# Optimization experiments

Measured on AMD Instinct MI355X. Metric: run time of the kernel, lower is better.

The kernel has to match this reference:

```python
import jax, jax.numpy as jnp
import numpy as np

B, S, D = 4, 2048, 1024

def setup_inputs() -> dict:
    key = jax.random.key(0)
    kv, kk, kq, kw = jax.random.split(key, 4)
    scale = 1.0 / np.sqrt(D)
    v = jax.random.normal(kv, (B, S, D), dtype=jnp.float32)
    k = jax.random.normal(kk, (B, S, D), dtype=jnp.float32)
    q = jax.random.normal(kq, (B, S, D), dtype=jnp.float32)
    wi = jax.random.normal(kw, (D, D), dtype=jnp.float32) * scale
    mask = jnp.tril(jnp.ones((S, S), dtype=bool))[None, :, :]  # causal [1,S,S]
    return {"v": v, "k": k, "q": q, "wi": wi, "mask": mask}

def reference(v, k, q, wi, mask):
    # project q, k, v with the shared weight wi
    q = q @ wi
    k = k @ wi
    v = v @ wi
    # scaled dot-product scores [B,S,S]
    scores = jnp.einsum('bqd,bkd->bqk', q, k) / jnp.sqrt(jnp.asarray(q.shape[-1], q.dtype))
    scores = jnp.where(mask, scores, jnp.asarray(-1e10, scores.dtype))
    attn = jax.nn.softmax(scores, axis=-1)
    # residual: q + attn @ v
    return q + jnp.einsum('bqk,bkd->bqd', attn, v)
```

## Files before the change

kernel.cpp:

```cpp
#include <hip/hip_runtime.h>
#include <hip/hip_bf16.h>

typedef __hip_bfloat16 bf16;
typedef short bf16x8 __attribute__((ext_vector_type(8)));
typedef float f32x4 __attribute__((ext_vector_type(4)));

#define HT 16384

__device__ __forceinline__ void gload16(const void* g, void* l) {
    __builtin_amdgcn_global_load_lds(
        (const __attribute__((address_space(1))) void*)g,
        (__attribute__((address_space(3))) void*)l, 16, 0, 0);
}

__device__ __forceinline__ void stage_half(char* lds, const bf16* src, int ld,
                                           int rowbase, int k0, int slotIdx,
                                           int tid)
{
    char* dst = lds + (size_t)slotIdx * HT + tid * 16;
    const int sub = tid >> 3;
    const int cb  = ((tid & 7) ^ (sub & 7)) << 4;
    #pragma unroll
    for (int p = 0; p < 2; ++p) {
        const int row = p * 64 + sub;
        const char* g = (const char*)(src + (size_t)(rowbase + row) * ld + k0) + cb;
        gload16(g, dst + p * 8192);
    }
}

__device__ __forceinline__ void stage_q(char* lds, const bf16* src, int ld,
                                        int rowbase, int k0, int slotIdx,
                                        int tid)
{
    char* dst = lds + (size_t)slotIdx * HT + tid * 16;
    #pragma unroll
    for (int p = 0; p < 4; ++p) {
        const int s = p * 256 + tid;
        const int row = s >> 3;
        const int cb = ((s & 7) ^ (row & 7)) << 4;
        const char* g = (const char*)(src + (size_t)(rowbase + row) * ld + k0) + cb;
        gload16(g, dst + p * 4096);
    }
}

__device__ __forceinline__ bf16x8 ldsfrag(const char* lds, int slotIdx,
                                          int row, int ks, int cb0)
{
    return *(const bf16x8*)(lds + (size_t)slotIdx * HT
                            + row * 128 + (cb0 ^ (ks << 6)));
}

__device__ __forceinline__ float bf2f(short s) {
    union { float f; unsigned u; } c;
    c.u = ((unsigned)(unsigned short)s) << 16;
    return c.f;
}

__launch_bounds__(512, 2)
__global__ void proj_2ph(const bf16* __restrict__ A, const bf16* __restrict__ B,
                         bf16* __restrict__ C)
{
    extern __shared__ char lds[];
    const int orig = blockIdx.y * 8 + blockIdx.x;
    const int wk2 = (orig & 7) * 96 + (orig >> 3);
    const int bi = wk2 >> 3, bj = wk2 & 7;
    const int brow = bi * 256, bcol = bj * 128;

    const int tid  = threadIdx.x;
    const int lane = tid & 63;
    const int w    = tid >> 6;
    const int wm   = w >> 1, wn = w & 1;
    const int fr   = lane & 15, fq = lane >> 4;
    const int cb0  = ((fr & 7) ^ fq) << 4;
    const int hA   = wm >> 1;
    const int rA   = (wm & 1) * 64;
    const int rB   = wn * 64;
    const int NT   = 16;

    f32x4 acc[4][4] = {};
    bf16x8 af[4][2], bv[4][2];

    stage_half(lds, A, 1024, brow,       0, 0, tid);
    stage_half(lds, A, 1024, brow + 128, 0, 1, tid);
    stage_half(lds, B, 1024, bcol,       0, 6, tid);
    stage_half(lds, A, 1024, brow,      64, 2, tid);
    stage_half(lds, A, 1024, brow + 128,64, 3, tid);
    stage_half(lds, B, 1024, bcol,     64, 7, tid);
    asm volatile("s_waitcnt vmcnt(6)" ::: "memory");
    __builtin_amdgcn_s_barrier();

#define MF8(n0)                                                               \
    _Pragma("unroll") for (int m = 0; m < 4; ++m)                             \
    _Pragma("unroll") for (int dn = 0; dn < 2; ++dn)                          \
    _Pragma("unroll") for (int ks = 0; ks < 2; ++ks)                          \
        acc[m][(n0)+dn] = __builtin_amdgcn_mfma_f32_16x16x32_bf16(            \
            af[m][ks], bv[(n0)+dn][ks], acc[m][(n0)+dn], 0, 0, 0);

    for (int t = 0; t < NT; ++t) {
        const int aslot = (t % 3) * 2 + hA;
        const int bslot = 6 + (t & 1);
        const int a2    = ((t + 2) % 3) * 2;
        const int k2    = min(t + 2, NT - 1) << 6;

        #pragma unroll
        for (int m = 0; m < 4; ++m)
            #pragma unroll
            for (int ks = 0; ks < 2; ++ks)
                af[m][ks] = ldsfrag(lds, aslot, rA + m * 16 + fr, ks, cb0);
        #pragma unroll
        for (int n = 0; n < 4; ++n)
            #pragma unroll
            for (int ks = 0; ks < 2; ++ks)
                bv[n][ks] = ldsfrag(lds, bslot, rB + n * 16 + fr, ks, cb0);
        stage_half(lds, A, 1024, brow,       k2, a2,     tid);
        stage_half(lds, A, 1024, brow + 128, k2, a2 + 1, tid);
        __builtin_amdgcn_s_barrier();
        __builtin_amdgcn_s_setprio(1);
        MF8(0)
        __builtin_amdgcn_s_setprio(0);
        __builtin_amdgcn_s_barrier();

        stage_half(lds, B, 1024, bcol, k2, bslot, tid);
        __builtin_amdgcn_s_barrier();
        __builtin_amdgcn_s_setprio(1);
        MF8(2)
        __builtin_amdgcn_s_setprio(0);
        asm volatile("s_waitcnt vmcnt(6)" ::: "memory");
        __builtin_amdgcn_s_barrier();
    }
#undef MF8

    #pragma unroll
    for (int mf = 0; mf < 4; ++mf) {
        const int r0 = brow + wm * 64 + mf * 16 + fq * 4;
        #pragma unroll
        for (int nf = 0; nf < 4; ++nf) {
            const int c = bcol + wn * 64 + nf * 16 + fr;
            #pragma unroll
            for (int j = 0; j < 4; ++j)
                C[(size_t)(r0 + j) * 1024 + c] = __float2bfloat16(acc[mf][nf][j]);
        }
    }
}

template<int MODE>
__device__ __forceinline__ void tile128v2(char* lds, const bf16* A, const bf16* B,
                                          bf16* Cb, float* Cf, const bf16* Res,
                                          int lda, int ldb, int ldcb,
                                          int brow, int bcol, int NT, float scale,
                                          int tid)
{
    const int lane = tid & 63;
    const int w    = tid >> 6;
    const int wm   = w >> 1, wn = w & 1;
    const int fr   = lane & 15, fq = lane >> 4;
    const int cb0  = ((fr & 7) ^ fq) << 4;

    f32x4 acc[4][4] = {};
    bf16x8 af[4][2], bv[4][2];

    stage_q(lds, A, lda, brow, 0,  0, tid);
    stage_q(lds, B, ldb, bcol, 0,  3, tid);
    stage_q(lds, A, lda, brow, 64, 1, tid);
    stage_q(lds, B, ldb, bcol, 64, 4, tid);
    asm volatile("s_waitcnt vmcnt(8)" ::: "memory");
    __builtin_amdgcn_s_barrier();

    for (int t = 0; t < NT; ++t) {
        const int aslot = t % 3, bslot = 3 + (t & 1);
        const int k2 = min(t + 2, NT - 1) << 6;

        #pragma unroll
        for (int m = 0; m < 4; ++m)
            #pragma unroll
            for (int ks = 0; ks < 2; ++ks)
                af[m][ks] = ldsfrag(lds, aslot, wm * 64 + m * 16 + fr, ks, cb0);
        #pragma unroll
        for (int n = 0; n < 4; ++n)
            #pragma unroll
            for (int ks = 0; ks < 2; ++ks)
                bv[n][ks] = ldsfrag(lds, bslot, wn * 64 + n * 16 + fr, ks, cb0);
        stage_q(lds, A, lda, brow, k2, (t + 2) % 3, tid);
        __builtin_amdgcn_s_barrier();
        __builtin_amdgcn_s_setprio(1);
        #pragma unroll
        for (int m = 0; m < 4; ++m)
            #pragma unroll
            for (int n = 0; n < 2; ++n)
                #pragma unroll
                for (int ks = 0; ks < 2; ++ks)
                    acc[m][n] = __builtin_amdgcn_mfma_f32_16x16x32_bf16(
                        af[m][ks], bv[n][ks], acc[m][n], 0, 0, 0);
        __builtin_amdgcn_s_setprio(0);
        __builtin_amdgcn_s_barrier();

        stage_q(lds, B, ldb, bcol, k2, bslot, tid);
        __builtin_amdgcn_s_barrier();
        __builtin_amdgcn_s_setprio(1);
        #pragma unroll
        for (int m = 0; m < 4; ++m)
            #pragma unroll
            for (int n = 2; n < 4; ++n)
                #pragma unroll
                for (int ks = 0; ks < 2; ++ks)
                    acc[m][n] = __builtin_amdgcn_mfma_f32_16x16x32_bf16(
                        af[m][ks], bv[n][ks], acc[m][n], 0, 0, 0);
        __builtin_amdgcn_s_setprio(0);
        asm volatile("s_waitcnt vmcnt(8)" ::: "memory");
        __builtin_amdgcn_s_barrier();
    }

    #pragma unroll
    for (int mf = 0; mf < 4; ++mf) {
        const int r0 = brow + wm * 64 + mf * 16 + fq * 4;
        #pragma unroll
        for (int nf = 0; nf < 4; ++nf) {
            const int c = bcol + wn * 64 + nf * 16 + fr;
            #pragma unroll
            for (int j = 0; j < 4; ++j) {
                if (MODE == 1)
                    Cb[(size_t)(r0 + j) * ldcb + c] =
                        __float2bfloat16(acc[mf][nf][j] * scale);
                else
                    Cf[(size_t)(r0 + j) * ldcb + c] = acc[mf][nf][j] +
                        __bfloat162float(Res[(size_t)(r0 + j) * ldcb + c]);
            }
        }
    }
}

__launch_bounds__(256, 2)
__global__ void scores128(const bf16* __restrict__ qp, const bf16* __restrict__ kp,
                          bf16* __restrict__ P)
{
    extern __shared__ char lds[];
    const int j = blockIdx.x;
    int bi = (int)((__fsqrt_rn(8.0f * j + 1.0f) - 1.0f) * 0.5f);
    while ((bi + 1) * (bi + 2) / 2 <= j) ++bi;
    while (bi * (bi + 1) / 2 > j) --bi;
    const int bj = j - bi * (bi + 1) / 2;
    const int bz = blockIdx.z;

    tile128v2<1>(lds,
                 qp + (size_t)bz * 2048 * 1024,
                 kp + (size_t)bz * 2048 * 1024,
                 P + (size_t)bz * 2048 * 2048, nullptr, nullptr,
                 1024, 1024, 2048,
                 bi * 128, bj * 128, 16, 0.03125f, threadIdx.x);
}

__launch_bounds__(256, 2)
__global__ void pv128(const bf16* __restrict__ P, const bf16* __restrict__ V,
                      const bf16* __restrict__ R, float* __restrict__ C)
{
    extern __shared__ char lds[];
    const int x  = blockIdx.x;
    const int u  = x & 255;
    const int bs = u & 7;
    const int bj = (u >> 3) & 7;
    const int bz = u >> 6;
    const int bi = (x >> 8) ? (15 - bs) : bs;

    tile128v2<2>(lds,
                 P + (size_t)bz * 2048 * 2048,
                 V + (size_t)bz * 1024 * 2048,
                 nullptr,
                 C + (size_t)bz * 2048 * 1024,
                 R + (size_t)bz * 2048 * 1024,
                 2048, 2048, 1024,
                 bi * 128, bj * 128, 2 * (bi + 1), 1.0f, threadIdx.x);
}

__global__ void convert_and_wi(const float* __restrict__ q,
                               const float* __restrict__ k,
                               const float* __restrict__ v,
                               const float* __restrict__ wi,
                               bf16* __restrict__ Xb, bf16* __restrict__ Wt)
{
    __shared__ float t[32][33];
    if (blockIdx.x < 1024) {
        const int n0 = (blockIdx.x & 31) * 32, k0 = (blockIdx.x >> 5) * 32;
        const int lx = threadIdx.x & 31, ly = threadIdx.x >> 5;
        for (int i = ly; i < 32; i += 8)
            t[i][lx] = wi[(size_t)(k0 + i) * 1024 + n0 + lx];
        __syncthreads();
        for (int i = ly; i < 32; i += 8)
            Wt[(size_t)(n0 + i) * 1024 + k0 + lx] = __float2bfloat16(t[lx][i]);
        return;
    }
    const int N8 = 8192 * 1024 / 8;
    const int total = 3 * N8;
    const int nconv = gridDim.x - 1024;
    for (int i = (blockIdx.x - 1024) * 256 + threadIdx.x; i < total;
         i += nconv * 256) {
        const int ti = i / N8, j = i - ti * N8;
        const float4* s = (ti == 0) ? (const float4*)q
                        : (ti == 1) ? (const float4*)k : (const float4*)v;
        float4 a = s[2 * j], bq = s[2 * j + 1];
        float vals[8] = {a.x, a.y, a.z, a.w, bq.x, bq.y, bq.z, bq.w};
        union { short h[8]; bf16x8 v8; } o;
        #pragma unroll
        for (int e = 0; e < 8; ++e) {
            bf16 hh = __float2bfloat16(vals[e]);
            o.h[e] = *(short*)&hh;
        }
        ((bf16x8*)Xb)[i] = o.v8;
    }
}

__global__ void transpose_vp(const bf16* __restrict__ vp, bf16* __restrict__ vpT)
{
    __shared__ bf16 t[32][33];
    const int b = blockIdx.z;
    const int d0 = blockIdx.x * 32, s0 = blockIdx.y * 32;
    const bf16* src = vp + (size_t)b * 2048 * 1024;
    bf16* dst = vpT + (size_t)b * 1024 * 2048;
    const int lx = threadIdx.x & 31, ly = threadIdx.x >> 5;
    for (int i = ly; i < 32; i += 8)
        t[i][lx] = src[(size_t)(s0 + i) * 1024 + d0 + lx];
    __syncthreads();
    for (int i = ly; i < 32; i += 8)
        dst[(size_t)(d0 + i) * 2048 + s0 + lx] = t[lx][i];
}

__launch_bounds__(256)
__global__ void softmax_rows(bf16* __restrict__ P)
{
    const int wid = threadIdx.x >> 6, lane = threadIdx.x & 63;
    const int r = blockIdx.x * 4 + wid, b = blockIdx.y;
    bf16* row = P + ((size_t)b * 2048 + r) * 2048;
    const int nv  = r + 1;
    const int rup = (r & ~127) + 128;

    float vals[4][8];
    float m = -1e30f;
    #pragma unroll
    for (int c = 0; c < 4; ++c) {
        const int k0 = c * 512 + lane * 8;
        if (k0 < rup) {
            bf16x8 x = *(const bf16x8*)(row + k0);
            #pragma unroll
            for (int j = 0; j < 8; ++j) {
                float f = (k0 + j < nv) ? bf2f(x[j]) : -1e30f;
                vals[c][j] = f;
                m = fmaxf(m, f);
            }
        } else {
            #pragma unroll
            for (int j = 0; j < 8; ++j) vals[c][j] = -1e30f;
        }
    }
    #pragma unroll
    for (int o = 32; o; o >>= 1) m = fmaxf(m, __shfl_xor(m, o));

    float sum = 0.f;
    #pragma unroll
    for (int c = 0; c < 4; ++c)
        #pragma unroll
        for (int j = 0; j < 8; ++j) {
            float e = __expf(vals[c][j] - m);
            vals[c][j] = e;
            sum += e;
        }
    #pragma unroll
    for (int o = 32; o; o >>= 1) sum += __shfl_xor(sum, o);
    const float inv = 1.0f / sum;

    #pragma unroll
    for (int c = 0; c < 4; ++c) {
        const int k0 = c * 512 + lane * 8;
        if (k0 < rup) {
            union { short h[8]; bf16x8 v8; } o;
            #pragma unroll
            for (int j = 0; j < 8; ++j) {
                bf16 hh = __float2bfloat16(vals[c][j] * inv);
                o.h[j] = *(short*)&hh;
            }
            *(bf16x8*)(row + k0) = o.v8;
        }
    }
}

extern "C" void kernel_launch(void* const* d_in, const int* in_sizes, int n_in,
                              void* d_out, int out_size, void* d_ws, size_t ws_size,
                              hipStream_t stream)
{
    const float* v  = (const float*)d_in[0];
    const float* k  = (const float*)d_in[1];
    const float* q  = (const float*)d_in[2];
    const float* wi = (const float*)d_in[3];
    float* out = (float*)d_out;

    char* ws = (char*)d_ws;
    const size_t WT_OFF   = 0;
    const size_t PROJ_OFF = WT_OFF + (2u << 20);
    const size_t VPT_OFF  = PROJ_OFF + (size_t)24576 * 1024 * 2;
    const size_t XB_OFF   = VPT_OFF + (size_t)4 * 1024 * 2048 * 2;

    bf16* Wt   = (bf16*)(ws + WT_OFF);
    bf16* proj = (bf16*)(ws + PROJ_OFF);
    bf16* vpT  = (bf16*)(ws + VPT_OFF);
    bf16* Xb   = (bf16*)(ws + XB_OFF);
    bf16* P    = Xb;

    bf16* qp_b = proj;
    bf16* kp_b = proj + (size_t)8192 * 1024;
    bf16* vp_b = proj + (size_t)16384 * 1024;

    (void)hipFuncSetAttribute((const void*)proj_2ph,
            hipFuncAttributeMaxDynamicSharedMemorySize, 131072);
    (void)hipFuncSetAttribute((const void*)scores128,
            hipFuncAttributeMaxDynamicSharedMemorySize, 81920);
    (void)hipFuncSetAttribute((const void*)pv128,
            hipFuncAttributeMaxDynamicSharedMemorySize, 81920);

    convert_and_wi<<<3072, 256, 0, stream>>>(q, k, v, wi, Xb, Wt);

    proj_2ph<<<dim3(8, 96), 512, 131072, stream>>>(Xb, Wt, proj);

    transpose_vp<<<dim3(32, 64, 4), 256, 0, stream>>>(vp_b, vpT);

    scores128<<<dim3(136, 1, 4), 256, 81920, stream>>>(qp_b, kp_b, P);

    softmax_rows<<<dim3(512, 4), 256, 0, stream>>>(P);

    pv128<<<dim3(512), 256, 81920, stream>>>(P, vpT, qp_b, out);
}
```

Baseline: 179.1 us.

## Reassociate attention with shared weight: precompute Wi·Wiᵀ and apply Wi after PV

Uses the shared projection to rewrite the math. Scores become q·(Wi Wiᵀ)·kᵀ, so only a 1024x1024 Gram product and one q projection are computed instead of projecting q, k and v. The output becomes (q + attn·v)·Wi, so the residual and PV run on raw inputs and a final GEMM applies Wi. This removes one of the three large projection GEMMs and the projected-v transpose, and the new transpose kernel converts v directly from fp32. The cost is an extra small GEMM and an extra intermediate Y rounded to bf16, which changes the rounding behaviour.

```diff
diff --git a/kernel.cpp b/kernel.cpp
--- a/kernel.cpp
+++ b/kernel.cpp
@@ -56,14 +56,18 @@
     return c.f;
 }
 
+template<int MODE>
 __launch_bounds__(512, 2)
-__global__ void proj_2ph(const bf16* __restrict__ A, const bf16* __restrict__ B,
-                         bf16* __restrict__ C)
+__global__ void gemm_a256(const bf16* __restrict__ A, const bf16* __restrict__ B,
+                          bf16* __restrict__ Cb, float* __restrict__ Cf)
 {
     extern __shared__ char lds[];
-    const int orig = blockIdx.y * 8 + blockIdx.x;
-    const int wk2 = (orig & 7) * 96 + (orig >> 3);
-    const int bi = wk2 >> 3, bj = wk2 & 7;
+    const int gx = gridDim.x;
+    const int nwg = gx * gridDim.y;
+    const int chunk = nwg >> 3;
+    const int orig = blockIdx.y * gx + blockIdx.x;
+    const int wk2 = (orig & 7) * chunk + (orig >> 3);
+    const int bi = wk2 / gx, bj = wk2 % gx;
     const int brow = bi * 256, bcol = bj * 128;
 
     const int tid  = threadIdx.x;
@@ -137,15 +141,20 @@
         for (int nf = 0; nf < 4; ++nf) {
             const int c = bcol + wn * 64 + nf * 16 + fr;
             #pragma unroll
-            for (int j = 0; j < 4; ++j)
-                C[(size_t)(r0 + j) * 1024 + c] = __float2bfloat16(acc[mf][nf][j]);
+            for (int j = 0; j < 4; ++j) {
+                if (MODE == 0)
+                    Cb[(size_t)(r0 + j) * 1024 + c] =
+                        __float2bfloat16(acc[mf][nf][j]);
+                else
+                    Cf[(size_t)(r0 + j) * 1024 + c] = acc[mf][nf][j];
+            }
         }
     }
 }
 
 template<int MODE>
 __device__ __forceinline__ void tile128v2(char* lds, const bf16* A, const bf16* B,
-                                          bf16* Cb, float* Cf, const bf16* Res,
+                                          bf16* Cb, const float* Rf,
                                           int lda, int ldb, int ldcb,
                                           int brow, int bcol, int NT, float scale,
                                           int tid)
@@ -222,15 +231,15 @@
                     Cb[(size_t)(r0 + j) * ldcb + c] =
                         __float2bfloat16(acc[mf][nf][j] * scale);
                 else
-                    Cf[(size_t)(r0 + j) * ldcb + c] = acc[mf][nf][j] +
-                        __bfloat162float(Res[(size_t)(r0 + j) * ldcb + c]);
+                    Cb[(size_t)(r0 + j) * ldcb + c] = __float2bfloat16(
+                        acc[mf][nf][j] + Rf[(size_t)(r0 + j) * ldcb + c]);
             }
         }
     }
 }
 
 __launch_bounds__(256, 2)
-__global__ void scores128(const bf16* __restrict__ qp, const bf16* __restrict__ kp,
+__global__ void scores128(const bf16* __restrict__ qG, const bf16* __restrict__ kb,
                           bf16* __restrict__ P)
 {
     extern __shared__ char lds[];
@@ -242,16 +251,16 @@
     const int bz = blockIdx.z;
 
     tile128v2<1>(lds,
-                 qp + (size_t)bz * 2048 * 1024,
-                 kp + (size_t)bz * 2048 * 1024,
-                 P + (size_t)bz * 2048 * 2048, nullptr, nullptr,
+                 qG + (size_t)bz * 2048 * 1024,
+                 kb + (size_t)bz * 2048 * 1024,
+                 P + (size_t)bz * 2048 * 2048, nullptr,
                  1024, 1024, 2048,
                  bi * 128, bj * 128, 16, 0.03125f, threadIdx.x);
 }
 
 __launch_bounds__(256, 2)
-__global__ void pv128(const bf16* __restrict__ P, const bf16* __restrict__ V,
-                      const bf16* __restrict__ R, float* __restrict__ C)
+__global__ void pv128(const bf16* __restrict__ P, const bf16* __restrict__ vT,
+                      const float* __restrict__ q, bf16* __restrict__ Y)
 {
     extern __shared__ char lds[];
     const int x  = blockIdx.x;
@@ -263,64 +272,65 @@
 
     tile128v2<2>(lds,
                  P + (size_t)bz * 2048 * 2048,
-                 V + (size_t)bz * 1024 * 2048,
-                 nullptr,
-                 C + (size_t)bz * 2048 * 1024,
-                 R + (size_t)bz * 2048 * 1024,
+                 vT + (size_t)bz * 1024 * 2048,
+                 Y + (size_t)bz * 2048 * 1024,
+                 q + (size_t)bz * 2048 * 1024,
                  2048, 2048, 1024,
                  bi * 128, bj * 128, 2 * (bi + 1), 1.0f, threadIdx.x);
 }
 
-__global__ void convert_and_wi(const float* __restrict__ q,
-                               const float* __restrict__ k,
-                               const float* __restrict__ v,
-                               const float* __restrict__ wi,
-                               bf16* __restrict__ Xb, bf16* __restrict__ Wt)
+__global__ void convert_qk_w(const float* __restrict__ q, const float* __restrict__ k,
+                             const float* __restrict__ wi,
+                             bf16* __restrict__ qb, bf16* __restrict__ kb,
+                             bf16* __restrict__ Wb)
+{
+    const int N8 = 8192 * 1024 / 8;
+    const int W8 = 1024 * 1024 / 8;
+    const int total = 2 * N8 + W8;
+    for (int i = blockIdx.x * 256 + threadIdx.x; i < total; i += gridDim.x * 256) {
+        const float4* s;
+        bf16* dst;
+        int j;
+        if (i < N8)            { s = (const float4*)q;  dst = qb; j = i; }
+        else if (i < 2 * N8)   { s = (const float4*)k;  dst = kb; j = i - N8; }
+        else                   { s = (const float4*)wi; dst = Wb; j = i - 2 * N8; }
+        float4 a = s[2 * j], b = s[2 * j + 1];
+        float vals[8] = {a.x, a.y, a.z, a.w, b.x, b.y, b.z, b.w};
+        union { short h[8]; bf16x8 v8; } o;
+        #pragma unroll
+        for (int e = 0; e < 8; ++e) {
+            bf16 hh = __float2bfloat16(vals[e]);
+            o.h[e] = *(short*)&hh;
+        }
+        ((bf16x8*)dst)[j] = o.v8;
+    }
+}
+
+__global__ void transpose_vwi(const float* __restrict__ v,
+                              const float* __restrict__ wi,
+                              bf16* __restrict__ vT, bf16* __restrict__ Wt)
 {
     __shared__ float t[32][33];
-    if (blockIdx.x < 1024) {
-        const int n0 = (blockIdx.x & 31) * 32, k0 = (blockIdx.x >> 5) * 32;
-        const int lx = threadIdx.x & 31, ly = threadIdx.x >> 5;
+    const int z = blockIdx.z;
+    const int lx = threadIdx.x & 31, ly = threadIdx.x >> 5;
+    if (z < 4) {
+        const int d0 = blockIdx.x * 32, s0 = blockIdx.y * 32;
+        const float* src = v + (size_t)z * 2048 * 1024;
+        bf16* dst = vT + (size_t)z * 1024 * 2048;
+        for (int i = ly; i < 32; i += 8)
+            t[i][lx] = src[(size_t)(s0 + i) * 1024 + d0 + lx];
+        __syncthreads();
+        for (int i = ly; i < 32; i += 8)
+            dst[(size_t)(d0 + i) * 2048 + s0 + lx] = __float2bfloat16(t[lx][i]);
+    } else {
+        if (blockIdx.y >= 32) return;
+        const int n0 = blockIdx.x * 32, k0 = blockIdx.y * 32;
         for (int i = ly; i < 32; i += 8)
             t[i][lx] = wi[(size_t)(k0 + i) * 1024 + n0 + lx];
         __syncthreads();
         for (int i = ly; i < 32; i += 8)
             Wt[(size_t)(n0 + i) * 1024 + k0 + lx] = __float2bfloat16(t[lx][i]);
-        return;
-    }
-    const int N8 = 8192 * 1024 / 8;
-    const int total = 3 * N8;
-    const int nconv = gridDim.x - 1024;
-    for (int i = (blockIdx.x - 1024) * 256 + threadIdx.x; i < total;
-         i += nconv * 256) {
-        const int ti = i / N8, j = i - ti * N8;
-        const float4* s = (ti == 0) ? (const float4*)q
-                        : (ti == 1) ? (const float4*)k : (const float4*)v;
-        float4 a = s[2 * j], bq = s[2 * j + 1];
-        float vals[8] = {a.x, a.y, a.z, a.w, bq.x, bq.y, bq.z, bq.w};
-        union { short h[8]; bf16x8 v8; } o;
-        #pragma unroll
-        for (int e = 0; e < 8; ++e) {
-            bf16 hh = __float2bfloat16(vals[e]);
-            o.h[e] = *(short*)&hh;
-        }
-        ((bf16x8*)Xb)[i] = o.v8;
-    }
-}
-
-__global__ void transpose_vp(const bf16* __restrict__ vp, bf16* __restrict__ vpT)
-{
-    __shared__ bf16 t[32][33];
-    const int b = blockIdx.z;
-    const int d0 = blockIdx.x * 32, s0 = blockIdx.y * 32;
-    const bf16* src = vp + (size_t)b * 2048 * 1024;
-    bf16* dst = vpT + (size_t)b * 1024 * 2048;
-    const int lx = threadIdx.x & 31, ly = threadIdx.x >> 5;
-    for (int i = ly; i < 32; i += 8)
-        t[i][lx] = src[(size_t)(s0 + i) * 1024 + d0 + lx];
-    __syncthreads();
-    for (int i = ly; i < 32; i += 8)
-        dst[(size_t)(d0 + i) * 2048 + s0 + lx] = t[lx][i];
+    }
 }
 
 __launch_bounds__(256)
@@ -392,37 +402,38 @@
     float* out = (float*)d_out;
 
     char* ws = (char*)d_ws;
-    const size_t WT_OFF   = 0;
-    const size_t PROJ_OFF = WT_OFF + (2u << 20);
-    const size_t VPT_OFF  = PROJ_OFF + (size_t)24576 * 1024 * 2;
-    const size_t XB_OFF   = VPT_OFF + (size_t)4 * 1024 * 2048 * 2;
-
-    bf16* Wt   = (bf16*)(ws + WT_OFF);
-    bf16* proj = (bf16*)(ws + PROJ_OFF);
-    bf16* vpT  = (bf16*)(ws + VPT_OFF);
-    bf16* Xb   = (bf16*)(ws + XB_OFF);
-    bf16* P    = Xb;
-
-    bf16* qp_b = proj;
-    bf16* kp_b = proj + (size_t)8192 * 1024;
-    bf16* vp_b = proj + (size_t)16384 * 1024;
-
-    (void)hipFuncSetAttribute((const void*)proj_2ph,
+    const size_t MB = 1u << 20;
+    bf16* Wb = (bf16*)(ws);
+    bf16* Wt = (bf16*)(ws + 2 * MB);
+    bf16* G  = (bf16*)(ws + 4 * MB);
+    bf16* qb = (bf16*)(ws + 6 * MB);
+    bf16* kb = (bf16*)(ws + 22 * MB);
+    bf16* vT = (bf16*)(ws + 38 * MB);
+    bf16* qG = (bf16*)(ws + 54 * MB);
+    bf16* Y  = (bf16*)(ws + 70 * MB);
+    bf16* P  = (bf16*)(ws + 86 * MB);
+
+    (void)hipFuncSetAttribute((const void*)gemm_a256<0>,
+            hipFuncAttributeMaxDynamicSharedMemorySize, 131072);
+    (void)hipFuncSetAttribute((const void*)gemm_a256<2>,
             hipFuncAttributeMaxDynamicSharedMemorySize, 131072);
     (void)hipFuncSetAttribute((const void*)scores128,
             hipFuncAttributeMaxDynamicSharedMemorySize, 81920);
     (void)hipFuncSetAttribute((const void*)pv128,
             hipFuncAttributeMaxDynamicSharedMemorySize, 81920);
 
-    convert_and_wi<<<3072, 256, 0, stream>>>(q, k, v, wi, Xb, Wt);
-
-    proj_2ph<<<dim3(8, 96), 512, 131072, stream>>>(Xb, Wt, proj);
-
-    transpose_vp<<<dim3(32, 64, 4), 256, 0, stream>>>(vp_b, vpT);
-
-    scores128<<<dim3(136, 1, 4), 256, 81920, stream>>>(qp_b, kp_b, P);
+    convert_qk_w<<<2048, 256, 0, stream>>>(q, k, wi, qb, kb, Wb);
+    transpose_vwi<<<dim3(32, 64, 5), 256, 0, stream>>>(v, wi, vT, Wt);
+
+    gemm_a256<0><<<dim3(8, 4), 512, 131072, stream>>>(Wb, Wb, G, nullptr);
+
+    gemm_a256<0><<<dim3(8, 32), 512, 131072, stream>>>(qb, G, qG, nullptr);
+
+    scores128<<<dim3(136, 1, 4), 256, 81920, stream>>>(qG, kb, P);
 
     softmax_rows<<<dim3(512, 4), 256, 0, stream>>>(P);
 
-    pv128<<<dim3(512), 256, 81920, stream>>>(P, vpT, qp_b, out);
-}
+    pv128<<<dim3(512), 256, 81920, stream>>>(P, vT, q, Y);
+
+    gemm_a256<2><<<dim3(8, 32), 512, 131072, stream>>>(Y, Wt, nullptr, out);
+}
```

Measured after the change: 173.9 us. -2.9%, faster.
